# Performance work log

Measured on AMD Instinct MI355X. Metric: run time of the kernel, lower is better.

The kernel has to match this reference:

```python
import jax, jax.numpy as jnp
import numpy as np

N_NODES = 100000
N_EDGES = 1600000
IN_DIM = 128
OUT_DIM = 128


def setup_inputs() -> dict:
    key = jax.random.key(0)
    ks = jax.random.split(key, 8)
    x = jax.random.normal(ks[0], (N_NODES, IN_DIM), dtype=jnp.float32)
    one_hot_h = jax.random.normal(ks[1], (N_NODES, OUT_DIM), dtype=jnp.float32)
    # three candidate-op linear transforms (in_dim -> out_dim)
    W0 = jax.random.normal(ks[2], (IN_DIM, OUT_DIM), dtype=jnp.float32) * 0.05
    W1 = jax.random.normal(ks[3], (IN_DIM, OUT_DIM), dtype=jnp.float32) * 0.05
    W2 = jax.random.normal(ks[4], (IN_DIM, OUT_DIM), dtype=jnp.float32) * 0.05
    # sparse mask_matrix in COO form: out[r] += v * H[c]
    mask_rows = jax.random.randint(ks[5], (N_EDGES,), 0, N_NODES, dtype=jnp.int32)
    mask_cols = jax.random.randint(ks[6], (N_EDGES,), 0, N_NODES, dtype=jnp.int32)
    mask_vals = jax.random.uniform(ks[7], (N_EDGES,), dtype=jnp.float32)
    return {"x": x, "one_hot_h": one_hot_h, "W0": W0, "W1": W1, "W2": W2,
            "mask_rows": mask_rows, "mask_cols": mask_cols, "mask_vals": mask_vals}


def reference(x, one_hot_h, W0, W1, W2, mask_rows, mask_cols, mask_vals):
    # Original: sum_k spmm(mask_matrix, op_k(x)) + spmm(mask_matrix, one_hot_h).
    # spmm is linear, so summing per-op outputs pre-aggregation is exact and
    # fuses K spmm launches into one sparse aggregation pass.
    H = x @ W0 + x @ W1 + x @ W2 + one_hot_h              # [N, out_dim]
    gathered = mask_vals[:, None] * H[mask_cols]          # [E, out_dim]
    out = jax.ops.segment_sum(gathered, mask_rows, num_segments=x.shape[0])
    return out
```

## Files before the change

### kernel.cpp

```cpp
#include <hip/hip_runtime.h>
#include <hip/hip_bf16.h>

#define N_NODES 100000
#define N_EDGES 1600000
#define DIM 128

#define NBIN 256
#define RPP  391
#define PCAP 8192
#define P1_BLOCKS 512
#define CHUNK (N_EDGES / P1_BLOCKS)

typedef unsigned int uint_t;
typedef unsigned short ushort_t;
typedef float f32x4 __attribute__((ext_vector_type(4)));
typedef __bf16 bf16x8 __attribute__((ext_vector_type(8)));

__device__ inline uint_t f2bf(float f) {
    uint_t u = __float_as_uint(f);
    return (u + 0x7FFFu + ((u >> 16) & 1u)) >> 16;
}
__device__ inline float bf2f(uint_t lo16) { return __uint_as_float(lo16 << 16); }

__global__ __launch_bounds__(256) void pass1_bin(
        const int* __restrict__ rows, const int* __restrict__ cols,
        const float* __restrict__ vals, int* __restrict__ psize,
        long long* __restrict__ slab,
        const float* __restrict__ W0, const float* __restrict__ W1,
        const float* __restrict__ W2, ushort_t* __restrict__ WT) {
    if (blockIdx.x >= P1_BLOCKS) {
        int i = (blockIdx.x - P1_BLOCKS) * 256 + threadIdx.x;
        if (i < DIM * DIM) {
            int m = i & 127, k = i >> 7;
            float s = W0[k * DIM + m] + W1[k * DIM + m] + W2[k * DIM + m];
            WT[m * DIM + k] = (ushort_t)f2bf(s);
        }
        return;
    }
    __shared__ int hist[NBIN];
    __shared__ int binoff[NBIN];
    __shared__ int resv[NBIN];
    __shared__ int curs[NBIN];
    __shared__ long long ebuf[CHUNK];
    __shared__ int edest[CHUNK];

    int t = threadIdx.x;
    int e0 = blockIdx.x * CHUNK;

    if (t < NBIN) hist[t] = 0;
    __syncthreads();

    for (int i = t; i < CHUNK; i += 256) {
        int r = rows[e0 + i];
        atomicAdd(&hist[r / RPP], 1);
    }
    __syncthreads();

    if (t < 64) {
        int b = t * 4;
        int v0 = hist[b], v1 = hist[b + 1], v2 = hist[b + 2], v3 = hist[b + 3];
        int s = v0 + v1 + v2 + v3;
        int incl = s;
#pragma unroll
        for (int d = 1; d < 64; d <<= 1) {
            int o = __shfl_up(incl, d, 64);
            if (t >= d) incl += o;
        }
        int excl = incl - s;
        binoff[b]     = excl;
        binoff[b + 1] = excl + v0;
        binoff[b + 2] = excl + v0 + v1;
        binoff[b + 3] = excl + v0 + v1 + v2;
    }
    __syncthreads();

    if (t < NBIN) {
        int len = hist[t];
        int r = (len > 0) ? atomicAdd(&psize[t], len) : 0;
        resv[t] = t * PCAP + r;
        curs[t] = binoff[t];
    }
    __syncthreads();

    for (int i = t; i < CHUNK; i += 256) {
        int   r = rows[e0 + i];
        int   c = cols[e0 + i];
        float v = vals[e0 + i];
        int b  = r / RPP;
        int lr = r - b * RPP;
        int pos = atomicAdd(&curs[b], 1);
        uint_t key = ((uint_t)lr << 17) | (uint_t)c;
        ebuf[pos]  = ((long long)__float_as_int(v) << 32) | (long long)key;
        edest[pos] = resv[b] + (pos - binoff[b]);
    }
    __syncthreads();

    for (int i = t; i < CHUNK; i += 256)
        slab[edest[i]] = ebuf[i];
}

__global__ __launch_bounds__(256) void pass2_sort(
        const long long* __restrict__ slab, const int* __restrict__ psize,
        int* __restrict__ off, long long* __restrict__ csr) {
    __shared__ int pb[NBIN + 1];
    __shared__ int cnt[RPP + 1];
    __shared__ int loff[RPP + 1];
    __shared__ int curs[RPP];
    __shared__ long long ebuf[PCAP];

    int p = blockIdx.x, t = threadIdx.x;

    if (t < 64) {
        int b = t * 4;
        int v0 = min(psize[b], PCAP),     v1 = min(psize[b + 1], PCAP);
        int v2 = min(psize[b + 2], PCAP), v3 = min(psize[b + 3], PCAP);
        int s = v0 + v1 + v2 + v3;
        int incl = s;
#pragma unroll
        for (int d = 1; d < 64; d <<= 1) {
            int o = __shfl_up(incl, d, 64);
            if (t >= d) incl += o;
        }
        int excl = incl - s;
        pb[b]     = excl;
        pb[b + 1] = excl + v0;
        pb[b + 2] = excl + v0 + v1;
        pb[b + 3] = excl + v0 + v1 + v2;
        if (t == 63) pb[NBIN] = incl;
    }
    for (int i = t; i < RPP + 1; i += 256) cnt[i] = 0;
    __syncthreads();

    int n = min(psize[p], PCAP);
    int base = pb[p];
    int rlo = p * RPP;
    int nrows = N_NODES - rlo; if (nrows > RPP) nrows = RPP;
    const long long* seg = slab + (long long)p * PCAP;

    if (p == NBIN - 1 && t == 0) off[N_NODES] = pb[NBIN];

    for (int i = t; i < n; i += 256) {
        uint_t key = (uint_t)(seg[i] & 0xFFFFFFFFll);
        atomicAdd(&cnt[key >> 17], 1);
    }
    __syncthreads();

    if (t < 64) {
        int b7 = t * 7;
        int v[7]; int s = 0;
#pragma unroll
        for (int k = 0; k < 7; ++k) {
            int idx = b7 + k;
            v[k] = (idx < RPP) ? cnt[idx] : 0;
            s += v[k];
        }
        int incl = s;
#pragma unroll
        for (int d = 1; d < 64; d <<= 1) {
            int o = __shfl_up(incl, d, 64);
            if (t >= d) incl += o;
        }
        int run = incl - s;
#pragma unroll
        for (int k = 0; k < 7; ++k) {
            int idx = b7 + k;
            if (idx < RPP) loff[idx] = run;
            run += v[k];
        }
    }
    __syncthreads();

    for (int i = t; i < nrows; i += 256) {
        curs[i] = loff[i];
        off[rlo + i] = base + loff[i];
    }
    __syncthreads();

    for (int i = t; i < n; i += 256) {
        long long ev = seg[i];
        uint_t key = (uint_t)(ev & 0xFFFFFFFFll);
        int lr = key >> 17;
        uint_t c = key & 0x1FFFFu;
        int pos = atomicAdd(&curs[lr], 1);
        ebuf[pos] = (long long)(((unsigned long long)ev & 0xFFFFFFFF00000000ull) | c);
    }
    __syncthreads();

    for (int i = t; i < n; i += 256)
        __builtin_nontemporal_store(ebuf[i], &csr[base + i]);
}

#define GROWS 64
#define XSTR 136
__global__ __launch_bounds__(256) void gemm_mfma(const float* __restrict__ x,
                                                 const float* __restrict__ oh,
                                                 const ushort_t* __restrict__ WT,
                                                 uint_t* __restrict__ H16) {
    __shared__ ushort_t xs[GROWS * XSTR];
    int tid = threadIdx.x;
    int wv = tid >> 6, l = tid & 63;
    int lr = l & 15, kg = l >> 4;
    int lrow = wv * 16 + lr;
    long long base_row = (long long)blockIdx.x * GROWS;
    long long hr = base_row + lrow;

    const f32x4* xg = (const f32x4*)x;
#pragma unroll
    for (int i = 0; i < 8; ++i) {
        int g = tid + i * 256;
        int row = g >> 5, c4 = g & 31;
        long long sr = base_row + row; if (sr >= N_NODES) sr = N_NODES - 1;
        f32x4 v = __builtin_nontemporal_load(xg + sr * 32 + c4);
        ushort_t* d = &xs[row * XSTR + c4 * 4];
        d[0] = (ushort_t)f2bf(v.x); d[1] = (ushort_t)f2bf(v.y);
        d[2] = (ushort_t)f2bf(v.z); d[3] = (ushort_t)f2bf(v.w);
    }
    __syncthreads();

    f32x4 acc[8] = {};
#pragma unroll
    for (int s = 0; s < 4; ++s) {
        bf16x8 b = *(const bf16x8*)&xs[lrow * XSTR + s * 32 + kg * 8];
#pragma unroll
        for (int mt = 0; mt < 8; ++mt) {
            bf16x8 a = *(const bf16x8*)&WT[(mt * 16 + lr) * DIM + s * 32 + kg * 8];
            acc[mt] = __builtin_amdgcn_mfma_f32_16x16x32_bf16(a, b, acc[mt], 0, 0, 0);
        }
    }
    __syncthreads();

    const f32x4* og = (const f32x4*)oh;
#pragma unroll
    for (int i = 0; i < 8; ++i) {
        int g = tid + i * 256;
        int row = g >> 5, c4 = g & 31;
        long long sr = base_row + row; if (sr >= N_NODES) sr = N_NODES - 1;
        f32x4 v = __builtin_nontemporal_load(og + sr * 32 + c4);
        ushort_t* d = &xs[row * XSTR + c4 * 4];
        d[0] = (ushort_t)f2bf(v.x); d[1] = (ushort_t)f2bf(v.y);
        d[2] = (ushort_t)f2bf(v.z); d[3] = (ushort_t)f2bf(v.w);
    }
    __syncthreads();

    if (hr < N_NODES) {
#pragma unroll
        for (int mt = 0; mt < 8; ++mt) {
            int c0 = mt * 16 + kg * 4;
            const uint_t* ow = (const uint_t*)&xs[lrow * XSTR + c0];
            uint_t w0 = ow[0], w1 = ow[1];
            float f0 = acc[mt].x + bf2f(w0 & 0xFFFFu);
            float f1 = acc[mt].y + bf2f(w0 >> 16);
            float f2 = acc[mt].z + bf2f(w1 & 0xFFFFu);
            float f3 = acc[mt].w + bf2f(w1 >> 16);
            uint2 pk;
            pk.x = f2bf(f0) | (f2bf(f1) << 16);
            pk.y = f2bf(f2) | (f2bf(f3) << 16);
            *(uint2*)&H16[(size_t)hr * (DIM / 2) + c0 / 2] = pk;
        }
    }
}

__global__ __launch_bounds__(256) void gather_kernel(const uint_t* __restrict__ H16,
                                                     const int* __restrict__ off,
                                                     const long long* __restrict__ csr,
                                                     float* __restrict__ out) {
    int tid  = threadIdx.x;
    int wave = tid >> 6;
    int lane = tid & 63;
    int grp  = lane >> 4;
    int il   = lane & 15;
    int wid  = blockIdx.x * 16 + wave * 4 + grp;

    int s = off[wid], e = off[wid + 1];
    float acc[8] = {};

#define ACC8(h, v)                                                            \
    acc[0] += (v) * bf2f((h).x & 0xFFFFu); acc[1] += (v) * bf2f((h).x >> 16); \
    acc[2] += (v) * bf2f((h).y & 0xFFFFu); acc[3] += (v) * bf2f((h).y >> 16); \
    acc[4] += (v) * bf2f((h).z & 0xFFFFu); acc[5] += (v) * bf2f((h).z >> 16); \
    acc[6] += (v) * bf2f((h).w & 0xFFFFu); acc[7] += (v) * bf2f((h).w >> 16);

    int p = s;
    for (; p + 3 < e; p += 4) {
        long long cv0 = __builtin_nontemporal_load(&csr[p]);
        long long cv1 = __builtin_nontemporal_load(&csr[p + 1]);
        long long cv2 = __builtin_nontemporal_load(&csr[p + 2]);
        long long cv3 = __builtin_nontemporal_load(&csr[p + 3]);
        uint4 h0 = *(const uint4*)&H16[(long long)(int)(cv0 & 0x1FFFF) * (DIM / 2) + il * 4];
        uint4 h1 = *(const uint4*)&H16[(long long)(int)(cv1 & 0x1FFFF) * (DIM / 2) + il * 4];
        uint4 h2 = *(const uint4*)&H16[(long long)(int)(cv2 & 0x1FFFF) * (DIM / 2) + il * 4];
        uint4 h3 = *(const uint4*)&H16[(long long)(int)(cv3 & 0x1FFFF) * (DIM / 2) + il * 4];
        float v0 = __int_as_float((int)(cv0 >> 32));
        float v1 = __int_as_float((int)(cv1 >> 32));
        float v2 = __int_as_float((int)(cv2 >> 32));
        float v3 = __int_as_float((int)(cv3 >> 32));
        ACC8(h0, v0) ACC8(h1, v1) ACC8(h2, v2) ACC8(h3, v3)
    }
    for (; p < e; ++p) {
        long long cv = __builtin_nontemporal_load(&csr[p]);
        float v = __int_as_float((int)(cv >> 32));
        uint4 h = *(const uint4*)&H16[(long long)(int)(cv & 0x1FFFF) * (DIM / 2) + il * 4];
        ACC8(h, v)
    }
#undef ACC8

    float* op = &out[(long long)wid * DIM + il * 8];
    f32x4 o0 = {acc[0], acc[1], acc[2], acc[3]};
    f32x4 o1 = {acc[4], acc[5], acc[6], acc[7]};
    __builtin_nontemporal_store(o0, (f32x4*)op);
    __builtin_nontemporal_store(o1, (f32x4*)(op + 4));
}

extern "C" void kernel_launch(void* const* d_in, const int* in_sizes, int n_in,
                              void* d_out, int out_size, void* d_ws, size_t ws_size,
                              hipStream_t stream) {
    const float* x    = (const float*)d_in[0];
    const float* oh   = (const float*)d_in[1];
    const float* W0   = (const float*)d_in[2];
    const float* W1   = (const float*)d_in[3];
    const float* W2   = (const float*)d_in[4];
    const int*   rows = (const int*)d_in[5];
    const int*   cols = (const int*)d_in[6];
    const float* vals = (const float*)d_in[7];
    float* out = (float*)d_out;

    char* p = (char*)d_ws;
    size_t oW    = 0;
    size_t oH    = oW + 64 * 1024;
    size_t oOff  = oH + (size_t)N_NODES * DIM * 2;
    size_t oPs   = oOff + (size_t)(N_NODES + 32) * 4;
    size_t oSlab = oPs + 4096;
    size_t oCsr  = oSlab + (size_t)NBIN * PCAP * 8;

    ushort_t*  WT    = (ushort_t*)(p + oW);
    uint_t*    H16   = (uint_t*)(p + oH);
    int*       off   = (int*)(p + oOff);
    int*       psize = (int*)(p + oPs);
    long long* slab  = (long long*)(p + oSlab);
    long long* csr   = (long long*)(p + oCsr);

    (void)hipMemsetAsync(psize, 0, NBIN * sizeof(int), stream);
    pass1_bin<<<P1_BLOCKS + 64, 256, 0, stream>>>(rows, cols, vals, psize, slab,
                                                  W0, W1, W2, WT);
    pass2_sort<<<NBIN, 256, 0, stream>>>(slab, psize, off, csr);
    gemm_mfma<<<(N_NODES + GROWS - 1) / GROWS, 256, 0, stream>>>(x, oh, WT, H16);
    gather_kernel<<<N_NODES / 16, 256, 0, stream>>>(H16, off, csr, out);
}
```

Before: 162.9 us.

## Double bin count, stage partition in LDS, scatter sorted edges directly to global

Doubles the number of row bins to 512 with half the rows and half the capacity per bin, so the sort pass launches twice as many smaller blocks and uses less LDS per block. Pass 2 now loads each partition once into LDS with nontemporal loads and reuses it for both counting and scattering, instead of reading global memory twice. Sorted edges are written straight to their final global CSR position rather than staged through LDS, which removes one barrier and a copy loop but makes the global stores uncoalesced. The smaller PCAP increases the risk of overflow on skewed bins, since counts are clamped at capacity.

Result: no change. 161.9 us (-0.7%).

```diff
diff --git a/kernel.cpp b/kernel.cpp
--- a/kernel.cpp
+++ b/kernel.cpp
@@ -5,9 +5,9 @@
 #define N_EDGES 1600000
 #define DIM 128
 
-#define NBIN 256
-#define RPP  391
-#define PCAP 8192
+#define NBIN 512
+#define RPP  196
+#define PCAP 4096
 #define P1_BLOCKS 512
 #define CHUNK (N_EDGES / P1_BLOCKS)
 
@@ -47,7 +47,7 @@
     int t = threadIdx.x;
     int e0 = blockIdx.x * CHUNK;
 
-    if (t < NBIN) hist[t] = 0;
+    for (int i = t; i < NBIN; i += 256) hist[i] = 0;
     __syncthreads();
 
     for (int i = t; i < CHUNK; i += 256) {
@@ -57,28 +57,27 @@
     __syncthreads();
 
     if (t < 64) {
-        int b = t * 4;
-        int v0 = hist[b], v1 = hist[b + 1], v2 = hist[b + 2], v3 = hist[b + 3];
-        int s = v0 + v1 + v2 + v3;
+        int b = t * 8;
+        int v[8]; int s = 0;
+#pragma unroll
+        for (int k = 0; k < 8; ++k) { v[k] = hist[b + k]; s += v[k]; }
         int incl = s;
 #pragma unroll
         for (int d = 1; d < 64; d <<= 1) {
             int o = __shfl_up(incl, d, 64);
             if (t >= d) incl += o;
         }
-        int excl = incl - s;
-        binoff[b]     = excl;
-        binoff[b + 1] = excl + v0;
-        binoff[b + 2] = excl + v0 + v1;
-        binoff[b + 3] = excl + v0 + v1 + v2;
-    }
-    __syncthreads();
-
-    if (t < NBIN) {
-        int len = hist[t];
-        int r = (len > 0) ? atomicAdd(&psize[t], len) : 0;
-        resv[t] = t * PCAP + r;
-        curs[t] = binoff[t];
+        int run = incl - s;
+#pragma unroll
+        for (int k = 0; k < 8; ++k) { binoff[b + k] = run; run += v[k]; }
+    }
+    __syncthreads();
+
+    for (int i = t; i < NBIN; i += 256) {
+        int len = hist[i];
+        int r = (len > 0) ? atomicAdd(&psize[i], len) : 0;
+        resv[i] = i * PCAP + r;
+        curs[i] = binoff[i];
     }
     __syncthreads();
 
@@ -111,21 +110,19 @@
     int p = blockIdx.x, t = threadIdx.x;
 
     if (t < 64) {
-        int b = t * 4;
-        int v0 = min(psize[b], PCAP),     v1 = min(psize[b + 1], PCAP);
-        int v2 = min(psize[b + 2], PCAP), v3 = min(psize[b + 3], PCAP);
-        int s = v0 + v1 + v2 + v3;
+        int b = t * 8;
+        int v[8]; int s = 0;
+#pragma unroll
+        for (int k = 0; k < 8; ++k) { v[k] = min(psize[b + k], PCAP); s += v[k]; }
         int incl = s;
 #pragma unroll
         for (int d = 1; d < 64; d <<= 1) {
             int o = __shfl_up(incl, d, 64);
             if (t >= d) incl += o;
         }
-        int excl = incl - s;
-        pb[b]     = excl;
-        pb[b + 1] = excl + v0;
-        pb[b + 2] = excl + v0 + v1;
-        pb[b + 3] = excl + v0 + v1 + v2;
+        int run = incl - s;
+#pragma unroll
+        for (int k = 0; k < 8; ++k) { pb[b + k] = run; run += v[k]; }
         if (t == 63) pb[NBIN] = incl;
     }
     for (int i = t; i < RPP + 1; i += 256) cnt[i] = 0;
@@ -134,23 +131,27 @@
     int n = min(psize[p], PCAP);
     int base = pb[p];
     int rlo = p * RPP;
-    int nrows = N_NODES - rlo; if (nrows > RPP) nrows = RPP;
+    int nrows = N_NODES - rlo;
+    if (nrows > RPP) nrows = RPP;
+    if (nrows < 0) nrows = 0;
     const long long* seg = slab + (long long)p * PCAP;
 
     if (p == NBIN - 1 && t == 0) off[N_NODES] = pb[NBIN];
 
     for (int i = t; i < n; i += 256) {
-        uint_t key = (uint_t)(seg[i] & 0xFFFFFFFFll);
+        long long ev = __builtin_nontemporal_load(&seg[i]);
+        ebuf[i] = ev;
+        uint_t key = (uint_t)(ev & 0xFFFFFFFFll);
         atomicAdd(&cnt[key >> 17], 1);
     }
     __syncthreads();
 
     if (t < 64) {
-        int b7 = t * 7;
-        int v[7]; int s = 0;
-#pragma unroll
-        for (int k = 0; k < 7; ++k) {
-            int idx = b7 + k;
+        int b4 = t * 4;
+        int v[4]; int s = 0;
+#pragma unroll
+        for (int k = 0; k < 4; ++k) {
+            int idx = b4 + k;
             v[k] = (idx < RPP) ? cnt[idx] : 0;
             s += v[k];
         }
@@ -162,8 +163,8 @@
         }
         int run = incl - s;
 #pragma unroll
-        for (int k = 0; k < 7; ++k) {
-            int idx = b7 + k;
+        for (int k = 0; k < 4; ++k) {
+            int idx = b4 + k;
             if (idx < RPP) loff[idx] = run;
             run += v[k];
         }
@@ -177,17 +178,13 @@
     __syncthreads();
 
     for (int i = t; i < n; i += 256) {
-        long long ev = seg[i];
+        long long ev = ebuf[i];
         uint_t key = (uint_t)(ev & 0xFFFFFFFFll);
         int lr = key >> 17;
         uint_t c = key & 0x1FFFFu;
         int pos = atomicAdd(&curs[lr], 1);
-        ebuf[pos] = (long long)(((unsigned long long)ev & 0xFFFFFFFF00000000ull) | c);
-    }
-    __syncthreads();
-
-    for (int i = t; i < n; i += 256)
-        __builtin_nontemporal_store(ebuf[i], &csr[base + i]);
+        csr[base + pos] = (long long)(((unsigned long long)ev & 0xFFFFFFFF00000000ull) | c);
+    }
 }
 
 #define GROWS 64
```
